# Optimization experiments

Hardware: AMD Instinct MI355X
Metric: run time of the kernel (lower is better)

## Reference

```python
import jax, jax.numpy as jnp
import numpy as np
import math

D_MODEL = 768
EXPAND = 2
D_INNER = D_MODEL * EXPAND  # 1536
D_CONV = 4
D_STATE = 16
DT_RANK = math.ceil(D_MODEL / 16)  # 48
B, L = 2, 2048
LN_EPS = 1e-5


def setup_inputs() -> dict:
    key = jax.random.key(0)
    ks = jax.random.split(key, 12)
    s = lambda fan_in: 1.0 / np.sqrt(fan_in)
    return {
        "x": jax.random.normal(ks[0], (B, L, D_MODEL), dtype=jnp.float32),
        "ln_w": jnp.ones((D_MODEL,), jnp.float32),
        "ln_b": jnp.zeros((D_MODEL,), jnp.float32),
        "in_proj_w": jax.random.normal(ks[1], (2 * D_INNER, D_MODEL), jnp.float32) * s(D_MODEL),
        "conv_w": jax.random.normal(ks[2], (D_INNER, D_CONV), jnp.float32) * s(D_CONV),
        "conv_b": jax.random.normal(ks[3], (D_INNER,), jnp.float32) * 0.01,
        "x_proj_w": jax.random.normal(ks[4], (DT_RANK + 2 * D_STATE, D_INNER), jnp.float32) * s(D_INNER),
        "dt_proj_w": jax.random.normal(ks[5], (D_INNER, DT_RANK), jnp.float32) * s(DT_RANK),
        "dt_proj_b": jax.random.normal(ks[6], (D_INNER,), jnp.float32) * 0.01,
        "A_log": jnp.log(jnp.broadcast_to(jnp.arange(1, D_STATE + 1, dtype=jnp.float32), (D_INNER, D_STATE))),
        "D": jnp.ones((D_INNER,), jnp.float32),
        "out_proj_w": jax.random.normal(ks[7], (D_MODEL, D_INNER), jnp.float32) * s(D_INNER),
    }


def _layernorm(x, w, b):
    mu = jnp.mean(x, axis=-1, keepdims=True)
    var = jnp.mean(jnp.square(x - mu), axis=-1, keepdims=True)
    return (x - mu) * jax.lax.rsqrt(var + LN_EPS) * w + b


def _selective_scan(u, delta, A, Bm, Cm, Dv):
    # u,delta: [b,l,d]; A: [d,n]; Bm,Cm: [b,l,n]; Dv: [d]
    deltaA = jnp.exp(delta[..., None] * A)               # [b,l,d,n]
    dBu = (delta * u)[..., None] * Bm[:, :, None, :]     # [b,l,d,n]
    b, l, d, n = deltaA.shape
    x0 = jnp.zeros((b, d, n), deltaA.dtype)

    def step(carry, inp):
        dA_i, dBu_i, C_i = inp                            # [b,d,n],[b,d,n],[b,n]
        x_new = dA_i * carry + dBu_i
        y_i = jnp.einsum('bdn,bn->bd', x_new, C_i)
        return x_new, y_i

    _, ys = jax.lax.scan(
        step, x0,
        (deltaA.transpose(1, 0, 2, 3), dBu.transpose(1, 0, 2, 3), Cm.transpose(1, 0, 2)))
    y = ys.transpose(1, 0, 2)                             # [b,l,d]
    return y + u * Dv


def reference(x, ln_w, ln_b, in_proj_w, conv_w, conv_b, x_proj_w,
              dt_proj_w, dt_proj_b, A_log, D, out_proj_w):
    residual = x
    h = _layernorm(x, ln_w, ln_b)
    xr = h @ in_proj_w.T                                  # [b,l,2*d_inner]
    u, res = jnp.split(xr, [D_INNER], axis=-1)
    # depthwise causal conv1d
    uc = u.transpose(0, 2, 1)                             # [b,d,l]
    uc = jax.lax.conv_general_dilated(
        uc, conv_w[:, None, :], window_strides=(1,),
        padding=[(D_CONV - 1, 0)],
        dimension_numbers=('NCH', 'OIH', 'NCH'),
        feature_group_count=D_INNER) + conv_b[None, :, None]
    u = jax.nn.silu(uc.transpose(0, 2, 1))                # [b,l,d]
    # SSM
    x_dbl = u @ x_proj_w.T
    dt, Bm, Cm = jnp.split(x_dbl, [DT_RANK, DT_RANK + D_STATE], axis=-1)
    delta = jax.nn.softplus(dt @ dt_proj_w.T + dt_proj_b)
    A = -jnp.exp(A_log)
    y = _selective_scan(u, delta, A, Bm, Cm, D)
    y = y * jax.nn.silu(res)
    return y @ out_proj_w.T + residual
```

## Files before the change

kernel.cpp:

```cpp
#include <hip/hip_runtime.h>

#define DEV __device__ __forceinline__

typedef __attribute__((ext_vector_type(8))) short bf16x8;
typedef __attribute__((ext_vector_type(4))) float f32x4;

#define BB 2
#define LL 2048
#define MM 4096
#define DMODEL 768
#define DINNER 1536
#define NSTATE 16
#define CH 32
#define NCH 64

DEV unsigned short f2b(float f) {
  unsigned int x = __float_as_uint(f);
  x += 0x7fffu + ((x >> 16) & 1u);
  return (unsigned short)(x >> 16);
}
DEV float b2f(unsigned short u) { return __uint_as_float(((unsigned int)u) << 16); }
DEV float silu_f(float v) { return v / (1.f + __expf(-v)); }

DEV void async16(void* lds, const void* g) {
  __builtin_amdgcn_global_load_lds(
      (const __attribute__((address_space(1))) unsigned int*)g,
      (__attribute__((address_space(3))) unsigned int*)lds, 16, 0, 0);
}

__global__ __launch_bounds__(256) void k_prep(const float* __restrict__ w_in,
                                              const float* __restrict__ w_out,
                                              const float* __restrict__ w_xp,
                                              const float* __restrict__ w_dt,
                                              const float* __restrict__ alog,
                                              unsigned short* __restrict__ winb,
                                              unsigned short* __restrict__ woutb,
                                              unsigned short* __restrict__ wxpb,
                                              unsigned short* __restrict__ wdtb,
                                              float* __restrict__ a2) {
  int bid = blockIdx.x, t = threadIdx.x;
  if (bid < 2304) {
    int i = bid * 256 + t;
    float4 v = ((const float4*)w_in)[i];
    ushort4 o; o.x = f2b(v.x); o.y = f2b(v.y); o.z = f2b(v.z); o.w = f2b(v.w);
    ((ushort4*)winb)[i] = o;
  } else if (bid < 3456) {
    int i = (bid - 2304) * 256 + t;
    float4 v = ((const float4*)w_out)[i];
    ushort4 o; o.x = f2b(v.x); o.y = f2b(v.y); o.z = f2b(v.z); o.w = f2b(v.w);
    ((ushort4*)woutb)[i] = o;
  } else if (bid < 4224) {
    int i = (bid - 3456) * 256 + t;
    wxpb[i] = (i < 80 * 1536) ? f2b(w_xp[i]) : (unsigned short)0;
  } else if (bid < 4608) {
    int i = (bid - 4224) * 256 + t;
    int row = i >> 6, col = i & 63;
    wdtb[i] = (col < 48) ? f2b(w_dt[row * 48 + col]) : (unsigned short)0;
  } else {
    int i = (bid - 4608) * 256 + t;
    a2[i] = -__expf(alog[i]) * 1.44269504088896f;
  }
}

__global__ __launch_bounds__(256) void k_ln(const float* __restrict__ x,
                                            const float* __restrict__ w,
                                            const float* __restrict__ b,
                                            unsigned short* __restrict__ h) {
  int row = blockIdx.x, tid = threadIdx.x;
  const float* xr = x + (size_t)row * DMODEL;
  float v0 = xr[tid], v1 = xr[tid + 256], v2 = xr[tid + 512];
  float s = v0 + v1 + v2;
  float s2 = v0 * v0 + v1 * v1 + v2 * v2;
#pragma unroll
  for (int o = 32; o > 0; o >>= 1) { s += __shfl_down(s, o); s2 += __shfl_down(s2, o); }
  __shared__ float ps[4], ps2[4];
  if ((tid & 63) == 0) { ps[tid >> 6] = s; ps2[tid >> 6] = s2; }
  __syncthreads();
  s = ps[0] + ps[1] + ps[2] + ps[3];
  s2 = ps2[0] + ps2[1] + ps2[2] + ps2[3];
  float mu = s * (1.f / DMODEL);
  float var = s2 * (1.f / DMODEL) - mu * mu;
  float rs = rsqrtf(var + 1e-5f);
  h[(size_t)row * DMODEL + tid]       = f2b((v0 - mu) * rs * w[tid] + b[tid]);
  h[(size_t)row * DMODEL + tid + 256] = f2b((v1 - mu) * rs * w[tid + 256] + b[tid + 256]);
  h[(size_t)row * DMODEL + tid + 512] = f2b((v2 - mu) * rs * w[tid + 512] + b[tid + 512]);
}

template <int EPI, int OBF>
__global__ __launch_bounds__(256) void k_gemm_bt(const unsigned short* __restrict__ A,
                                                 const unsigned short* __restrict__ B,
                                                 float* __restrict__ C,
                                                 unsigned short* __restrict__ Cb,
                                                 int M, int N, int Kst, int KC,
                                                 const float* __restrict__ aux) {
  __shared__ unsigned short lA[128 * 32];
  __shared__ unsigned short lB[128 * 32];
  const int tid = threadIdx.x;
  const int bm = blockIdx.x * 128;
  const int bn = blockIdx.y * 128;
  const int lane = tid & 63;
  const int w = tid >> 6;
  const int wr = (w >> 1) * 64;
  const int wc = (w & 1) * 64;

  f32x4 acc[4][4];
#pragma unroll
  for (int i = 0; i < 4; ++i)
#pragma unroll
    for (int j = 0; j < 4; ++j) acc[i][j] = (f32x4)(0.0f);

  const int srow = tid >> 2;
  const int kc = (tid & 3) * 8;
  const int k0 = blockIdx.z * KC;

  for (int kt = k0; kt < k0 + KC; kt += 32) {
#pragma unroll
    for (int s = 0; s < 2; ++s) {
      int row = s * 64 + srow;
      int f = s * 256 + tid;
      async16(&lA[f * 8], A + (size_t)(bm + row) * Kst + kt + kc);
      async16(&lB[f * 8], B + (size_t)(bn + row) * Kst + kt + kc);
    }
    __syncthreads();
    const int ll = lane & 15, lh = (lane >> 4) * 8;
    bf16x8 af[4], bfr[4];
#pragma unroll
    for (int mi = 0; mi < 4; ++mi) af[mi] = *(const bf16x8*)&lA[(wr + mi * 16 + ll) * 32 + lh];
#pragma unroll
    for (int ni = 0; ni < 4; ++ni) bfr[ni] = *(const bf16x8*)&lB[(wc + ni * 16 + ll) * 32 + lh];
#pragma unroll
    for (int mi = 0; mi < 4; ++mi)
#pragma unroll
      for (int ni = 0; ni < 4; ++ni)
        acc[mi][ni] = __builtin_amdgcn_mfma_f32_16x16x32_bf16(af[mi], bfr[ni], acc[mi][ni], 0, 0, 0);
    __syncthreads();
  }

  const size_t zoff = (size_t)blockIdx.z * M * N;
  const int ll = lane & 15, lh4 = (lane >> 4) * 4;
#pragma unroll
  for (int mi = 0; mi < 4; ++mi) {
#pragma unroll
    for (int ni = 0; ni < 4; ++ni) {
      int col = bn + wc + ni * 16 + ll;
#pragma unroll
      for (int q = 0; q < 4; ++q) {
        int row = bm + wr + mi * 16 + lh4 + q;
        size_t idx = (size_t)row * N + col;
        float v = acc[mi][ni][q];
        if (EPI == 1) { v += aux[col]; v = (v > 20.f) ? v : __logf(1.f + __expf(v)); }
        if (EPI == 2) { v += aux[idx]; }
        if (OBF) Cb[idx] = f2b(v);
        else C[zoff + idx] = v;
      }
    }
  }
}

__global__ __launch_bounds__(128) void k_xpj_fin(const float* __restrict__ part,
                                                 float* __restrict__ xdbl,
                                                 unsigned short* __restrict__ dtb) {
  int row = blockIdx.x, t = threadIdx.x;
  size_t idx = (size_t)row * 128 + t;
  float s = 0.f;
#pragma unroll
  for (int p = 0; p < 4; ++p) s += part[(size_t)p * MM * 128 + idx];
  xdbl[idx] = s;
  if (t < 64) dtb[row * 64 + t] = (t < 48) ? f2b(s) : (unsigned short)0;
}

__global__ __launch_bounds__(256) void k_conv(const unsigned short* __restrict__ xrb,
                                              const float* __restrict__ cw,
                                              const float* __restrict__ cb,
                                              unsigned short* __restrict__ ub) {
  int i = blockIdx.x * 256 + threadIdx.x;
  int d4 = i % (DINNER / 4);
  int m = i / (DINNER / 4);
  int l = m & (LL - 1);
  const f32x4* cw4 = (const f32x4*)cw;
  f32x4 w0 = cw4[d4 * 4 + 0], w1 = cw4[d4 * 4 + 1];
  f32x4 w2 = cw4[d4 * 4 + 2], w3 = cw4[d4 * 4 + 3];
  f32x4 acc = ((const f32x4*)cb)[d4];
#pragma unroll
  for (int j = 0; j < 4; ++j) {
    if (l - 3 + j >= 0) {
      ushort4 in = ((const ushort4*)(xrb + (size_t)(m - 3 + j) * 3072))[d4];
      f32x4 iv;
      iv[0] = b2f(in.x); iv[1] = b2f(in.y); iv[2] = b2f(in.z); iv[3] = b2f(in.w);
      f32x4 wj;
      wj[0] = w0[j]; wj[1] = w1[j]; wj[2] = w2[j]; wj[3] = w3[j];
      acc += iv * wj;
    }
  }
  ushort4 ob;
  ob.x = f2b(silu_f(acc[0])); ob.y = f2b(silu_f(acc[1]));
  ob.z = f2b(silu_f(acc[2])); ob.w = f2b(silu_f(acc[3]));
  ((ushort4*)ub)[i] = ob;
}

__global__ __launch_bounds__(256) void k_scan1(const unsigned short* __restrict__ deltab,
                                               const unsigned short* __restrict__ ub,
                                               const float* __restrict__ xdbl,
                                               const float* __restrict__ a2g,
                                               float* __restrict__ P, float* __restrict__ S) {
  __shared__ unsigned short sd[CH * 256];
  __shared__ unsigned short su[CH * 256];
  int bid = blockIdx.x;
  int dblk = bid % 6;
  int c = (bid / 6) % NCH;
  int b = bid / (6 * NCH);
  int t = threadIdx.x;
  int d0 = dblk * 256, d = d0 + t;
  size_t mbase = (size_t)b * LL + c * CH;
#pragma unroll
  for (int i = 0; i < 4; ++i) {
    int o = i * 256 + t, r = o >> 5, l = o & 31;
    async16(&sd[r * 256 + l * 8], deltab + (mbase + r) * DINNER + d0 + l * 8);
    async16(&su[r * 256 + l * 8], ub + (mbase + r) * DINNER + d0 + l * 8);
  }
  f32x4 a2v[4], xs[4], pr[4];
  const f32x4* ga = (const f32x4*)(a2g + (size_t)d * 16);
#pragma unroll
  for (int q = 0; q < 4; ++q) { a2v[q] = ga[q]; xs[q] = (f32x4)(0.f); pr[q] = (f32x4)(1.f); }
  __syncthreads();

#pragma unroll 4
  for (int s = 0; s < CH; ++s) {
    float dt = b2f(sd[s * 256 + t]);
    float du = dt * b2f(su[s * 256 + t]);
    const f32x4* gb = (const f32x4*)(xdbl + (mbase + s) * 128 + 48);
#pragma unroll
    for (int q = 0; q < 4; ++q) {
      f32x4 bv = gb[q];
      f32x4 e = dt * a2v[q];
      f32x4 dA;
#pragma unroll
      for (int k = 0; k < 4; ++k) dA[k] = __builtin_amdgcn_exp2f(e[k]);
      xs[q] = dA * xs[q] + du * bv;
      pr[q] = pr[q] * dA;
    }
  }
  size_t base = (size_t)(b * NCH + c) * (16 * DINNER) + d;
#pragma unroll
  for (int q = 0; q < 4; ++q)
#pragma unroll
    for (int k = 0; k < 4; ++k) {
      P[base + (size_t)(q * 4 + k) * DINNER] = pr[q][k];
      S[base + (size_t)(q * 4 + k) * DINNER] = xs[q][k];
    }
}

__global__ __launch_bounds__(256) void k_scan2(float* __restrict__ P, const float* __restrict__ S) {
  int i = blockIdx.x * 256 + threadIdx.x;
  int b = i / (DINNER * 16);
  int j = i % (DINNER * 16);
  const size_t cs = (size_t)DINNER * 16;
  float* Pp = P + (size_t)b * NCH * cs + j;
  const float* Sp = S + (size_t)b * NCH * cs + j;
  float p0[8], s0[8], p1[8], s1[8];
#pragma unroll
  for (int k = 0; k < 8; ++k) { p0[k] = Pp[(size_t)k * cs]; s0[k] = Sp[(size_t)k * cs]; }
#pragma unroll
  for (int k = 0; k < 8; ++k) { p1[k] = Pp[(size_t)(8 + k) * cs]; s1[k] = Sp[(size_t)(8 + k) * cs]; }
  float carry = 0.f;
  for (int g = 0; g < NCH / 8; ++g) {
    float np[8], ns[8];
#pragma unroll
    for (int k = 0; k < 8; ++k) { np[k] = 0.f; ns[k] = 0.f; }
    if (g + 2 < NCH / 8) {
#pragma unroll
      for (int k = 0; k < 8; ++k) {
        np[k] = Pp[(size_t)((g + 2) * 8 + k) * cs];
        ns[k] = Sp[(size_t)((g + 2) * 8 + k) * cs];
      }
    }
#pragma unroll
    for (int k = 0; k < 8; ++k) {
      float tmp = carry;
      carry = fmaf(p0[k], carry, s0[k]);
      Pp[(size_t)(g * 8 + k) * cs] = tmp;
    }
#pragma unroll
    for (int k = 0; k < 8; ++k) { p0[k] = p1[k]; s0[k] = s1[k]; p1[k] = np[k]; s1[k] = ns[k]; }
  }
}

__global__ __launch_bounds__(256) void k_scan3(const unsigned short* __restrict__ deltab,
                                               const unsigned short* __restrict__ ub,
                                               const float* __restrict__ xdbl,
                                               const float* __restrict__ a2g,
                                               const float* __restrict__ P,
                                               const float* __restrict__ Dv,
                                               const unsigned short* __restrict__ xrb,
                                               unsigned short* __restrict__ yb) {
  __shared__ unsigned short sd[CH * 256];
  __shared__ unsigned short su[CH * 256];
  int bid = blockIdx.x;
  int dblk = bid % 6;
  int c = (bid / 6) % NCH;
  int b = bid / (6 * NCH);
  int t = threadIdx.x;
  int d0 = dblk * 256, d = d0 + t;
  size_t mbase = (size_t)b * LL + c * CH;
#pragma unroll
  for (int i = 0; i < 4; ++i) {
    int o = i * 256 + t, r = o >> 5, l = o & 31;
    async16(&sd[r * 256 + l * 8], deltab + (mbase + r) * DINNER + d0 + l * 8);
    async16(&su[r * 256 + l * 8], ub + (mbase + r) * DINNER + d0 + l * 8);
  }
  f32x4 a2v[4], xs[4];
  const f32x4* ga = (const f32x4*)(a2g + (size_t)d * 16);
#pragma unroll
  for (int q = 0; q < 4; ++q) a2v[q] = ga[q];
  size_t base = (size_t)(b * NCH + c) * (16 * DINNER) + d;
#pragma unroll
  for (int q = 0; q < 4; ++q)
#pragma unroll
    for (int k = 0; k < 4; ++k) xs[q][k] = P[base + (size_t)(q * 4 + k) * DINNER];
  float dval = Dv[d];
  __syncthreads();

#pragma unroll 4
  for (int s = 0; s < CH; ++s) {
    size_t m = mbase + s;
    float dt = b2f(sd[s * 256 + t]);
    float uv = b2f(su[s * 256 + t]);
    float du = dt * uv;
    const f32x4* gb = (const f32x4*)(xdbl + m * 128 + 48);
    const f32x4* gc = (const f32x4*)(xdbl + m * 128 + 64);
    f32x4 yv = (f32x4)(0.f);
#pragma unroll
    for (int q = 0; q < 4; ++q) {
      f32x4 bv = gb[q], cv = gc[q];
      f32x4 e = dt * a2v[q];
      f32x4 dA;
#pragma unroll
      for (int k = 0; k < 4; ++k) dA[k] = __builtin_amdgcn_exp2f(e[k]);
      xs[q] = dA * xs[q] + du * bv;
      yv += xs[q] * cv;
    }
    float y = yv[0] + yv[1] + yv[2] + yv[3] + uv * dval;
    float res = b2f(xrb[m * 3072 + DINNER + d]);
    y *= silu_f(res);
    yb[m * DINNER + d] = f2b(y);
  }
}

extern "C" void kernel_launch(void* const* d_in, const int* in_sizes, int n_in,
                              void* d_out, int out_size, void* d_ws, size_t ws_size,
                              hipStream_t stream) {
  const float* x     = (const float*)d_in[0];
  const float* ln_w  = (const float*)d_in[1];
  const float* ln_b  = (const float*)d_in[2];
  const float* w_in  = (const float*)d_in[3];
  const float* cw    = (const float*)d_in[4];
  const float* cb    = (const float*)d_in[5];
  const float* w_xp  = (const float*)d_in[6];
  const float* w_dt  = (const float*)d_in[7];
  const float* b_dt  = (const float*)d_in[8];
  const float* alog  = (const float*)d_in[9];
  const float* Dv    = (const float*)d_in[10];
  const float* w_out = (const float*)d_in[11];
  float* out = (float*)d_out;

  char* ws = (char*)d_ws;
  unsigned short* h_b    = (unsigned short*)(ws + 0);
  unsigned short* winb   = (unsigned short*)(ws + 6291456);
  unsigned short* woutb  = (unsigned short*)(ws + 11010048);
  unsigned short* wxpb   = (unsigned short*)(ws + 13369344);
  unsigned short* wdtb   = (unsigned short*)(ws + 13762560);
  float*          a2     = (float*)(ws + 13959168);
  unsigned short* xrb    = (unsigned short*)(ws + 14057472);
  unsigned short* ub     = (unsigned short*)(ws + 39223296);
  float*          xpart  = (float*)(ws + 51806208);
  float*          xdbl   = (float*)(ws + 60194816);
  unsigned short* dtb    = (unsigned short*)(ws + 62291968);
  unsigned short* deltab = (unsigned short*)(ws + 62816256);
  float*          P      = (float*)(ws + 75399168);
  float*          S      = (float*)(ws + 87982080);
  unsigned short* yb     = (unsigned short*)(ws + 100564992);

  k_prep<<<4704, 256, 0, stream>>>(w_in, w_out, w_xp, w_dt, alog, winb, woutb, wxpb, wdtb, a2);

  k_ln<<<MM, 256, 0, stream>>>(x, ln_w, ln_b, h_b);

  k_gemm_bt<0, 1><<<dim3(32, 24, 1), 256, 0, stream>>>(h_b, winb, nullptr, xrb, MM, 3072, 768, 768, nullptr);

  k_conv<<<(MM * (DINNER / 4)) / 256, 256, 0, stream>>>(xrb, cw, cb, ub);

  k_gemm_bt<0, 0><<<dim3(32, 1, 4), 256, 0, stream>>>(ub, wxpb, xpart, nullptr, MM, 128, 1536, 384, nullptr);
  k_xpj_fin<<<MM, 128, 0, stream>>>(xpart, xdbl, dtb);

  k_gemm_bt<1, 1><<<dim3(32, 12, 1), 256, 0, stream>>>(dtb, wdtb, nullptr, deltab, MM, DINNER, 64, 64, b_dt);

  k_scan1<<<BB * NCH * 6, 256, 0, stream>>>(deltab, ub, xdbl, a2, P, S);
  k_scan2<<<(BB * DINNER * 16) / 256, 256, 0, stream>>>(P, S);
  k_scan3<<<BB * NCH * 6, 256, 0, stream>>>(deltab, ub, xdbl, a2, P, Dv, xrb, yb);

  k_gemm_bt<2, 0><<<dim3(32, 6, 1), 256, 0, stream>>>(yb, woutb, out, nullptr, MM, DMODEL, 1536, 1536, x);
}
```

Baseline: 176.2 us.

## Swizzle GEMM LDS layout and split-K the x_proj and out_proj GEMMs

Applies an XOR swizzle to the LDS tile layout in the generic GEMM to cut bank conflicts on fragment loads. The x_proj GEMM now splits K eight ways instead of four. The out_proj GEMM moves to a new 64-row-tile kernel with two-way split-K, and a separate finalize kernel sums the partials and adds the residual. This gives more blocks to fill the GPU, at the cost of extra partial-sum memory traffic and one more kernel launch.

```diff
diff --git a/kernel.cpp b/kernel.cpp
--- a/kernel.cpp
+++ b/kernel.cpp
@@ -110,7 +110,7 @@
     for (int j = 0; j < 4; ++j) acc[i][j] = (f32x4)(0.0f);
 
   const int srow = tid >> 2;
-  const int kc = (tid & 3) * 8;
+  const int sg = ((tid & 3) ^ ((srow >> 2) & 3)) * 8;
   const int k0 = blockIdx.z * KC;
 
   for (int kt = k0; kt < k0 + KC; kt += 32) {
@@ -118,16 +118,22 @@
     for (int s = 0; s < 2; ++s) {
       int row = s * 64 + srow;
       int f = s * 256 + tid;
-      async16(&lA[f * 8], A + (size_t)(bm + row) * Kst + kt + kc);
-      async16(&lB[f * 8], B + (size_t)(bn + row) * Kst + kt + kc);
+      async16(&lA[f * 8], A + (size_t)(bm + row) * Kst + kt + sg);
+      async16(&lB[f * 8], B + (size_t)(bn + row) * Kst + kt + sg);
     }
     __syncthreads();
-    const int ll = lane & 15, lh = (lane >> 4) * 8;
+    const int ll = lane & 15, sl = lane >> 4;
     bf16x8 af[4], bfr[4];
 #pragma unroll
-    for (int mi = 0; mi < 4; ++mi) af[mi] = *(const bf16x8*)&lA[(wr + mi * 16 + ll) * 32 + lh];
-#pragma unroll
-    for (int ni = 0; ni < 4; ++ni) bfr[ni] = *(const bf16x8*)&lB[(wc + ni * 16 + ll) * 32 + lh];
+    for (int mi = 0; mi < 4; ++mi) {
+      int row = wr + mi * 16 + ll;
+      af[mi] = *(const bf16x8*)&lA[row * 32 + ((sl ^ ((row >> 2) & 3)) * 8)];
+    }
+#pragma unroll
+    for (int ni = 0; ni < 4; ++ni) {
+      int row = wc + ni * 16 + ll;
+      bfr[ni] = *(const bf16x8*)&lB[row * 32 + ((sl ^ ((row >> 2) & 3)) * 8)];
+    }
 #pragma unroll
     for (int mi = 0; mi < 4; ++mi)
 #pragma unroll
@@ -149,9 +155,78 @@
         size_t idx = (size_t)row * N + col;
         float v = acc[mi][ni][q];
         if (EPI == 1) { v += aux[col]; v = (v > 20.f) ? v : __logf(1.f + __expf(v)); }
-        if (EPI == 2) { v += aux[idx]; }
         if (OBF) Cb[idx] = f2b(v);
         else C[zoff + idx] = v;
+      }
+    }
+  }
+}
+
+__global__ __launch_bounds__(256) void k_gemm64(const unsigned short* __restrict__ A,
+                                                const unsigned short* __restrict__ B,
+                                                float* __restrict__ C,
+                                                int M, int N, int Kst, int KC) {
+  __shared__ unsigned short lA[64 * 32];
+  __shared__ unsigned short lB[128 * 32];
+  const int tid = threadIdx.x;
+  const int bm = blockIdx.x * 64;
+  const int bn = blockIdx.y * 128;
+  const int lane = tid & 63;
+  const int w = tid >> 6;
+  const int wr = (w >> 1) * 32;
+  const int wc = (w & 1) * 64;
+
+  f32x4 acc[2][4];
+#pragma unroll
+  for (int i = 0; i < 2; ++i)
+#pragma unroll
+    for (int j = 0; j < 4; ++j) acc[i][j] = (f32x4)(0.0f);
+
+  const int srow = tid >> 2;
+  const int sg = ((tid & 3) ^ ((srow >> 2) & 3)) * 8;
+  const int k0 = blockIdx.z * KC;
+
+  for (int kt = k0; kt < k0 + KC; kt += 32) {
+    async16(&lA[tid * 8], A + (size_t)(bm + srow) * Kst + kt + sg);
+#pragma unroll
+    for (int i = 0; i < 2; ++i) {
+      int f = i * 256 + tid;
+      int r = f >> 2;
+      int g = ((f & 3) ^ ((r >> 2) & 3)) * 8;
+      async16(&lB[f * 8], B + (size_t)(bn + r) * Kst + kt + g);
+    }
+    __syncthreads();
+    const int ll = lane & 15, sl = lane >> 4;
+    bf16x8 af[2], bfr[4];
+#pragma unroll
+    for (int mi = 0; mi < 2; ++mi) {
+      int row = wr + mi * 16 + ll;
+      af[mi] = *(const bf16x8*)&lA[row * 32 + ((sl ^ ((row >> 2) & 3)) * 8)];
+    }
+#pragma unroll
+    for (int ni = 0; ni < 4; ++ni) {
+      int row = wc + ni * 16 + ll;
+      bfr[ni] = *(const bf16x8*)&lB[row * 32 + ((sl ^ ((row >> 2) & 3)) * 8)];
+    }
+#pragma unroll
+    for (int mi = 0; mi < 2; ++mi)
+#pragma unroll
+      for (int ni = 0; ni < 4; ++ni)
+        acc[mi][ni] = __builtin_amdgcn_mfma_f32_16x16x32_bf16(af[mi], bfr[ni], acc[mi][ni], 0, 0, 0);
+    __syncthreads();
+  }
+
+  const size_t zoff = (size_t)blockIdx.z * M * N;
+  const int ll = lane & 15, lh4 = (lane >> 4) * 4;
+#pragma unroll
+  for (int mi = 0; mi < 2; ++mi) {
+#pragma unroll
+    for (int ni = 0; ni < 4; ++ni) {
+      int col = bn + wc + ni * 16 + ll;
+#pragma unroll
+      for (int q = 0; q < 4; ++q) {
+        int row = bm + wr + mi * 16 + lh4 + q;
+        C[zoff + (size_t)row * N + col] = acc[mi][ni][q];
       }
     }
   }
@@ -164,9 +239,19 @@
   size_t idx = (size_t)row * 128 + t;
   float s = 0.f;
 #pragma unroll
-  for (int p = 0; p < 4; ++p) s += part[(size_t)p * MM * 128 + idx];
+  for (int p = 0; p < 8; ++p) s += part[(size_t)p * MM * 128 + idx];
   xdbl[idx] = s;
   if (t < 64) dtb[row * 64 + t] = (t < 48) ? f2b(s) : (unsigned short)0;
+}
+
+__global__ __launch_bounds__(256) void k_opj_fin(const float* __restrict__ part,
+                                                 const float* __restrict__ x,
+                                                 float* __restrict__ out) {
+  int i = blockIdx.x * 256 + threadIdx.x;
+  f32x4 a = ((const f32x4*)part)[i];
+  f32x4 b = ((const f32x4*)(part + (size_t)MM * DMODEL))[i];
+  f32x4 r = ((const f32x4*)x)[i];
+  ((f32x4*)out)[i] = a + b + r;
 }
 
 __global__ __launch_bounds__(256) void k_conv(const unsigned short* __restrict__ xrb,
@@ -373,12 +458,13 @@
   unsigned short* xrb    = (unsigned short*)(ws + 14057472);
   unsigned short* ub     = (unsigned short*)(ws + 39223296);
   float*          xpart  = (float*)(ws + 51806208);
-  float*          xdbl   = (float*)(ws + 60194816);
-  unsigned short* dtb    = (unsigned short*)(ws + 62291968);
-  unsigned short* deltab = (unsigned short*)(ws + 62816256);
-  float*          P      = (float*)(ws + 75399168);
-  float*          S      = (float*)(ws + 87982080);
-  unsigned short* yb     = (unsigned short*)(ws + 100564992);
+  float*          xdbl   = (float*)(ws + 68583424);
+  unsigned short* dtb    = (unsigned short*)(ws + 70680576);
+  unsigned short* deltab = (unsigned short*)(ws + 71204864);
+  float*          P      = (float*)(ws + 83787776);
+  float*          S      = (float*)(ws + 96370688);
+  unsigned short* yb     = (unsigned short*)(ws + 108953600);
+  float*          opart  = (float*)(ws + 121536512);
 
   k_prep<<<4704, 256, 0, stream>>>(w_in, w_out, w_xp, w_dt, alog, winb, woutb, wxpb, wdtb, a2);
 
@@ -388,7 +474,7 @@
 
   k_conv<<<(MM * (DINNER / 4)) / 256, 256, 0, stream>>>(xrb, cw, cb, ub);
 
-  k_gemm_bt<0, 0><<<dim3(32, 1, 4), 256, 0, stream>>>(ub, wxpb, xpart, nullptr, MM, 128, 1536, 384, nullptr);
+  k_gemm_bt<0, 0><<<dim3(32, 1, 8), 256, 0, stream>>>(ub, wxpb, xpart, nullptr, MM, 128, 1536, 192, nullptr);
   k_xpj_fin<<<MM, 128, 0, stream>>>(xpart, xdbl, dtb);
 
   k_gemm_bt<1, 1><<<dim3(32, 12, 1), 256, 0, stream>>>(dtb, wdtb, nullptr, deltab, MM, DINNER, 64, 64, b_dt);
@@ -397,5 +483,6 @@
   k_scan2<<<(BB * DINNER * 16) / 256, 256, 0, stream>>>(P, S);
   k_scan3<<<BB * NCH * 6, 256, 0, stream>>>(deltab, ub, xdbl, a2, P, Dv, xrb, yb);
 
-  k_gemm_bt<2, 0><<<dim3(32, 6, 1), 256, 0, stream>>>(yb, woutb, out, nullptr, MM, DMODEL, 1536, 1536, x);
-}
+  k_gemm64<<<dim3(64, 6, 2), 256, 0, stream>>>(yb, woutb, opart, MM, DMODEL, 1536, 768);
+  k_opj_fin<<<(MM * DMODEL / 4) / 256, 256, 0, stream>>>(opart, x, out);
+}
```

Measured after the change: 164.8 us. 1.07x faster.
